# Kernel optimization log

Measured on AMD Instinct MI355X. Metric: run time of the kernel, lower is better.

## Reference

```python
import jax, jax.numpy as jnp
import numpy as np

NUM_USER = 30000
NUM_ITEM = 30000
N = NUM_USER + NUM_ITEM
DIM = 64          # dim_latent
HID = 4 * DIM     # MLP hidden = 4*dim_latent
E_PAIRS = 500000  # user-item interactions; symmetrized -> 2*E_PAIRS edges
K = 10            # sampling (user-graph neighbors)
B = 2048          # batch_size
DV, DA, DT = 1024, 128, 100


def setup_inputs() -> dict:
    key = jax.random.key(0)
    ks = jax.random.split(key, 24)
    src = jax.random.randint(ks[0], (E_PAIRS,), 0, NUM_USER)
    dst = jax.random.randint(ks[1], (E_PAIRS,), NUM_USER, N)
    # symmetrize like torch.cat((edge, edge[[1,0]]), dim=1)
    edge_index = jnp.stack([jnp.concatenate([src, dst]),
                            jnp.concatenate([dst, src])])  # [2, 2*E_PAIRS]

    def lin_w(k, o, i):
        s = 1.0 / np.sqrt(i)
        return jax.random.uniform(k, (o, i), minval=-s, maxval=s, dtype=jnp.float32)

    return {
        "user_nodes": jax.random.randint(ks[2], (B,), 0, NUM_USER),
        "pos_item_nodes": jax.random.randint(ks[3], (B,), NUM_USER, N),
        "neg_item_nodes": jax.random.randint(ks[4], (B,), NUM_USER, N),
        "user_graph": jax.random.randint(ks[5], (NUM_USER, K), 0, NUM_USER),
        "edge_index": edge_index,
        "user_weight_matrix": jax.nn.softmax(jax.random.normal(ks[6], (NUM_USER, K), dtype=jnp.float32), axis=-1),
        "v_feat": jax.random.normal(ks[7], (NUM_ITEM, DV), dtype=jnp.float32),
        "a_feat": jax.random.normal(ks[8], (NUM_ITEM, DA), dtype=jnp.float32),
        "t_feat": jax.random.normal(ks[9], (NUM_ITEM, DT), dtype=jnp.float32),
        "v_pref": 0.1 * jax.random.normal(ks[10], (NUM_USER, DIM), dtype=jnp.float32),
        "a_pref": 0.1 * jax.random.normal(ks[11], (NUM_USER, DIM), dtype=jnp.float32),
        "t_pref": 0.1 * jax.random.normal(ks[12], (NUM_USER, DIM), dtype=jnp.float32),
        "v_W1": lin_w(ks[13], HID, DV), "v_b1": jnp.zeros((HID,), jnp.float32),
        "v_W2": lin_w(ks[14], DIM, HID), "v_b2": jnp.zeros((DIM,), jnp.float32),
        "a_W1": lin_w(ks[15], HID, DA), "a_b1": jnp.zeros((HID,), jnp.float32),
        "a_W2": lin_w(ks[16], DIM, HID), "a_b2": jnp.zeros((DIM,), jnp.float32),
        "t_W1": lin_w(ks[17], HID, DT), "t_b1": jnp.zeros((HID,), jnp.float32),
        "t_W2": lin_w(ks[18], DIM, HID), "t_b2": jnp.zeros((DIM,), jnp.float32),
        "weight_u": jax.nn.softmax(jax.random.normal(ks[19], (NUM_USER, 3, 1), dtype=jnp.float32), axis=1),
    }


def _l2norm(x):
    # F.normalize(x): rowwise L2 with eps=1e-12
    return x / jnp.maximum(jnp.linalg.norm(x, axis=-1, keepdims=True), 1e-12)


def _gcn_conv(x, src, dst, dinv):
    # Base_gcn(aggr='add'): out[i] = sum_{e: dst_e=i} dinv[src_e]*dinv[dst_e]*x[src_e]
    norm = dinv[src] * dinv[dst]
    return jax.ops.segment_sum(norm[:, None] * x[src], dst, num_segments=N)


def _modality(feat, pref, W1, b1, W2, b2, src, dst, dinv):
    # GCN.forward (Movielens branch, dim_latent=64)
    temp = jax.nn.leaky_relu(feat @ W1.T + b1) @ W2.T + b2  # MLP_1(leaky_relu(MLP(f)))
    x = _l2norm(jnp.concatenate([pref, temp], axis=0))       # [N, DIM]
    h = _gcn_conv(x, src, dst, dinv)
    h1 = _gcn_conv(h, src, dst, dinv)
    return h + x + h1


def reference(user_nodes, pos_item_nodes, neg_item_nodes, user_graph, edge_index,
              user_weight_matrix, v_feat, a_feat, t_feat,
              v_pref, a_pref, t_pref,
              v_W1, v_b1, v_W2, v_b2,
              a_W1, a_b1, a_W2, a_b2,
              t_W1, t_b1, t_W2, t_b2, weight_u):
    src, dst = edge_index[0], edge_index[1]
    deg = jax.ops.segment_sum(jnp.ones_like(src, dtype=jnp.float32), src, num_segments=N)
    dinv = jnp.where(deg > 0, deg ** -0.5, 0.0)

    v_rep = _modality(v_feat, v_pref, v_W1, v_b1, v_W2, v_b2, src, dst, dinv)
    a_rep = _modality(a_feat, a_pref, a_W1, a_b1, a_W2, a_b2, src, dst, dinv)
    t_rep = _modality(t_feat, t_pref, t_W1, t_b1, t_W2, t_b2, src, dst, dinv)

    representation = (v_rep + a_rep + t_rep) / 3.0
    # weighted_sum construction: per-user learned modality weights [U,3,1]
    user_stack = jnp.stack([v_rep[:NUM_USER], a_rep[:NUM_USER], t_rep[:NUM_USER]], axis=2)  # [U, D, 3]
    user_rep = jnp.einsum('udm,umo->ud', user_stack, weight_u)
    item_rep = representation[NUM_USER:]

    # User_Graph_sample: weighted sum over k sampled user neighbors
    h_u1 = jnp.einsum('uk,ukd->ud', user_weight_matrix, user_rep[user_graph])
    user_rep = user_rep + h_u1

    result = jnp.concatenate([user_rep, item_rep], axis=0)  # [N, DIM]
    u = result[user_nodes]
    pos_scores = jnp.sum(u * result[pos_item_nodes], axis=1)
    neg_scores = jnp.sum(u * result[neg_item_nodes], axis=1)
    return pos_scores, neg_scores
```

## Files before the change

### kernel.cpp

```cpp
#include <hip/hip_runtime.h>
#include <hip/hip_bf16.h>
#include <math.h>

#define NUSER 30000
#define NITEM 30000
#define NN    60000
#define NE    1000000
#define DIMV  64
#define XW    192
#define HIDW  256
#define NB    2048
#define KNB   10
#define MPAD  30080
#define NCH   235

typedef __attribute__((ext_vector_type(8))) short bf16x8;
typedef __attribute__((ext_vector_type(4))) float f32x4;

__device__ __forceinline__ short f2bf(float f) {
    union { float f; unsigned u; } v; v.f = f;
    unsigned r = v.u + 0x7fff + ((v.u >> 16) & 1);
    return (short)(r >> 16);
}
__device__ __forceinline__ float bflo(unsigned v) { return __int_as_float(v << 16); }
__device__ __forceinline__ float bfhi(unsigned v) { return __int_as_float(v & 0xffff0000u); }
__device__ __forceinline__ unsigned pack2(float a, float b) {
    return (unsigned)(unsigned short)f2bf(a) | ((unsigned)(unsigned short)f2bf(b) << 16);
}
__device__ __forceinline__ void async16(void* lds, const void* g) {
    __builtin_amdgcn_global_load_lds(
        (const __attribute__((address_space(1))) unsigned*)g,
        (__attribute__((address_space(3))) unsigned*)lds, 16, 0, 0);
}

__global__ void k_deg(const int* __restrict__ src, unsigned* __restrict__ deg) {
    int e = blockIdx.x * blockDim.x + threadIdx.x;
    if (e < NE) atomicAdd(&deg[src[e]], 1u);
}
__global__ void k_dinv(const unsigned* __restrict__ deg, float* __restrict__ dinv) {
    int i = blockIdx.x * blockDim.x + threadIdx.x;
    if (i < NN) { unsigned d = deg[i]; dinv[i] = d ? rsqrtf((float)d) : 0.f; }
}
__global__ __launch_bounds__(256)
void k_bsum(const unsigned* __restrict__ deg, int* __restrict__ bsum) {
    __shared__ int red[4];
    int g = blockIdx.x * 256 + threadIdx.x;
    int v = (g < NN) ? (int)deg[g] : 0;
    for (int o = 32; o > 0; o >>= 1) v += __shfl_down(v, o);
    int lane = threadIdx.x & 63, wave = threadIdx.x >> 6;
    if (lane == 0) red[wave] = v;
    __syncthreads();
    if (threadIdx.x == 0) bsum[blockIdx.x] = red[0] + red[1] + red[2] + red[3];
}
__global__ __launch_bounds__(256)
void k_bscan(const int* __restrict__ bsum, int* __restrict__ bscan) {
    __shared__ int s[256];
    int t = threadIdx.x;
    int v = (t < NCH) ? bsum[t] : 0;
    s[t] = v;
    __syncthreads();
    for (int o = 1; o < 256; o <<= 1) {
        int u = (t >= o) ? s[t - o] : 0;
        __syncthreads();
        s[t] += u;
        __syncthreads();
    }
    if (t < NCH) bscan[t] = s[t] - v;
}
__global__ __launch_bounds__(256)
void k_rowptr(const unsigned* __restrict__ deg, const int* __restrict__ bscan,
              int* __restrict__ rowptr) {
    __shared__ int s[256];
    int g = blockIdx.x * 256 + threadIdx.x, t = threadIdx.x;
    int v = (g < NN) ? (int)deg[g] : 0;
    s[t] = v;
    __syncthreads();
    for (int o = 1; o < 256; o <<= 1) {
        int u = (t >= o) ? s[t - o] : 0;
        __syncthreads();
        s[t] += u;
        __syncthreads();
    }
    int base = bscan[blockIdx.x];
    if (g < NN) rowptr[g] = base + s[t] - v;
    if (g == NN - 1) rowptr[NN] = base + s[t];
}
__global__ void k_fill(const int* __restrict__ src, const int* __restrict__ dst,
                       const float* __restrict__ dinv, const int* __restrict__ rowptr,
                       unsigned* __restrict__ cursor, int2* __restrict__ csr) {
    int e = blockIdx.x * blockDim.x + threadIdx.x;
    if (e >= NE) return;
    int s = src[e], d = dst[e];
    int pos = (int)atomicAdd(&cursor[d], 1u);
    int2 ew;
    ew.x = s;
    ew.y = __float_as_int(dinv[s] * dinv[d]);
    csr[rowptr[d] + pos] = ew;
}

struct CvtArgs { const float* src[6]; short* dst[6]; };
__constant__ __device__ const int C8PRE[7]  = {0,32768,36864,40960,43008,45056,47104};
__constant__ __device__ const int C8SH[6]   = {7,4,4,5,5,5};
__constant__ __device__ const int C8COLS[6] = {1024,128,100,256,256,256};
__constant__ __device__ const int C8ROWS[6] = {256,256,256,64,64,64};
#define CVT8_TOTAL 47104

__global__ __launch_bounds__(256)
void k_convert(CvtArgs a) {
    int cid = blockIdx.x * 256 + threadIdx.x;
    if (cid >= CVT8_TOTAL) return;
    int j = 0;
    while (cid >= C8PRE[j + 1]) ++j;
    int local = cid - C8PRE[j];
    int sh = C8SH[j];
    int r = local >> sh;
    int col = (local & ((1 << sh) - 1)) * 8;
    int cols = C8COLS[j];
    bf16x8 o = (bf16x8)0;
    if (r < C8ROWS[j]) {
        const float* s = a.src[j] + (size_t)r * cols + col;
        if (col + 8 <= cols) {
            float4 f0 = *(const float4*)s;
            float4 f1 = *(const float4*)(s + 4);
            o[0] = f2bf(f0.x); o[1] = f2bf(f0.y); o[2] = f2bf(f0.z); o[3] = f2bf(f0.w);
            o[4] = f2bf(f1.x); o[5] = f2bf(f1.y); o[6] = f2bf(f1.z); o[7] = f2bf(f1.w);
        } else {
            #pragma unroll
            for (int q = 0; q < 8; ++q)
                if (col + q < cols) o[q] = f2bf(s[q]);
        }
    }
    *(bf16x8*)(a.dst[j] + ((size_t)r << (sh + 3)) + col) = o;
}

__device__ __forceinline__ bf16x8 ldfrag(const short* lds, int row, int kbyte) {
    int off = (row * 128 + kbyte) ^ ((row & 7) << 4);
    return *(const bf16x8*)((const char*)lds + off);
}
__device__ __forceinline__ bf16x8 ldfrag512(const short* lds, int row, int kbyte) {
    int off = (row * 512 + kbyte) ^ ((row & 7) << 4);
    return *(const bf16x8*)((const char*)lds + off);
}
#define STAGE_TILE512(SMEM, BASEPTR, LDK, ROWOFF, K0, NITERS)                       \
    _Pragma("unroll")                                                                \
    for (int i_ = 0; i_ < (NITERS); ++i_) {                                          \
        int c_ = i_ * 512 + tid;                                                     \
        int r_ = c_ >> 3, slot_ = c_ & 7;                                            \
        int ss_ = slot_ ^ (r_ & 7);                                                  \
        const char* gp_ = (const char*)((BASEPTR) + (size_t)((ROWOFF) + r_) * (LDK)  \
                                        + (K0)) + ss_ * 16;                          \
        async16(&(SMEM)[c_ * 8], gp_);                                               \
    }

struct G12Args { const float* A[3]; const short* W1[3]; const float* b1[3];
                 const short* W2[3]; const float* b2[3]; int K[3]; int Ksrc[3]; };
__global__ __launch_bounds__(512)
void gemm12_mfma(G12Args g, float* __restrict__ X, short* __restrict__ Xb) {
    __shared__ __align__(16) float sAf[64 * 64];
    __shared__ __align__(16) short sB[256 * 64];
    short* sHid = sB;
    int m = blockIdx.z;
    int K  = g.K[m];
    int Ks = g.Ksrc[m];
    const float* A  = g.A[m];
    const short* W1 = g.W1[m];
    int tid = threadIdx.x;
    int lane = tid & 63, wave = tid >> 6;
    int wr2 = wave & 1, wc2 = wave >> 1;
    int lane15 = lane & 15, lhi = lane >> 4;
    int row0 = blockIdx.x * 64;
    int nt = K >> 6;
    f32x4 acc[2][4] = {};
    for (int t = 0; t < nt; ++t) {
        int k0 = t * 64;
        #pragma unroll
        for (int i_ = 0; i_ < 2; ++i_) {
            int c_ = i_ * 512 + tid;
            int r_ = c_ >> 4, slot = c_ & 15;
            int ss = slot ^ (r_ & 7);
            int grow = row0 + r_;
            if (grow >= NITEM) grow = NITEM - 1;
            int col = k0 + ss * 4;
            if (col + 4 > Ks) col = 0;
            async16(&sAf[c_ * 4], A + (size_t)grow * Ks + col);
        }
        STAGE_TILE512(sB, W1, K, 0, k0, 4)
        __syncthreads();
        #pragma unroll
        for (int ks = 0; ks < 2; ++ks) {
            bf16x8 a[2], b[4];
            #pragma unroll
            for (int mi = 0; mi < 2; ++mi) {
                int row = wr2 * 32 + mi * 16 + lane15;
                int cb = (ks * 32 + lhi * 8) * 4;
                int base = row * 256;
                int sw = (row & 7) << 4;
                f32x4 lo = *(const f32x4*)((const char*)sAf + ((base + cb) ^ sw));
                f32x4 hi = *(const f32x4*)((const char*)sAf + ((base + cb + 16) ^ sw));
                unsigned p0, p1, p2, p3;
                asm("v_cvt_pk_bf16_f32 %0, %1, %2" : "=v"(p0) : "v"(lo.x), "v"(lo.y));
                asm("v_cvt_pk_bf16_f32 %0, %1, %2" : "=v"(p1) : "v"(lo.z), "v"(lo.w));
                asm("v_cvt_pk_bf16_f32 %0, %1, %2" : "=v"(p2) : "v"(hi.x), "v"(hi.y));
                asm("v_cvt_pk_bf16_f32 %0, %1, %2" : "=v"(p3) : "v"(hi.z), "v"(hi.w));
                union { unsigned u[4]; bf16x8 v; } cvt;
                cvt.u[0] = p0; cvt.u[1] = p1; cvt.u[2] = p2; cvt.u[3] = p3;
                a[mi] = cvt.v;
            }
            int kb = ks * 64 + lhi * 16;
            #pragma unroll
            for (int ni = 0; ni < 4; ++ni) b[ni] = ldfrag(sB, wc2 * 64 + ni * 16 + lane15, kb);
            #pragma unroll
            for (int mi = 0; mi < 2; ++mi)
                #pragma unroll
                for (int ni = 0; ni < 4; ++ni)
                    acc[mi][ni] = __builtin_amdgcn_mfma_f32_16x16x32_bf16(a[mi], b[ni], acc[mi][ni], 0, 0, 0);
        }
        __syncthreads();
    }
    const float* b1 = g.b1[m];
    #pragma unroll
    for (int mi = 0; mi < 2; ++mi) {
        int rh0 = wr2 * 32 + mi * 16 + lhi * 4;
        #pragma unroll
        for (int ni = 0; ni < 4; ++ni) {
            int ch = wc2 * 64 + ni * 16 + lane15;
            float bv = b1[ch];
            #pragma unroll
            for (int r = 0; r < 4; ++r) {
                float v = acc[mi][ni][r] + bv;
                v = v > 0.f ? v : 0.01f * v;
                int rh = rh0 + r;
                int off = (rh * 512 + ch * 2) ^ ((rh & 7) << 4);
                *(short*)((char*)sHid + off) = f2bf(v);
            }
        }
    }
    __syncthreads();
    if (wave < 4) {
        const short* W2 = g.W2[m];
        const short* bp2 = W2 + (size_t)lane15 * HIDW + lhi * 8;
        f32x4 acc2[4] = {};
        #pragma unroll
        for (int k0 = 0; k0 < HIDW; k0 += 32) {
            bf16x8 a2 = ldfrag512(sHid, wave * 16 + lane15, k0 * 2 + lhi * 16);
            #pragma unroll
            for (int ni = 0; ni < 4; ++ni) {
                bf16x8 b2 = *(const bf16x8*)(bp2 + (size_t)ni * 16 * HIDW + k0);
                acc2[ni] = __builtin_amdgcn_mfma_f32_16x16x32_bf16(a2, b2, acc2[ni], 0, 0, 0);
            }
        }
        const float* b2 = g.b2[m];
        float v2[4][4];
        float sumsq[4] = {};
        #pragma unroll
        for (int ni = 0; ni < 4; ++ni) {
            float bv = b2[ni * 16 + lane15];
            #pragma unroll
            for (int r = 0; r < 4; ++r) {
                float x = acc2[ni][r] + bv;
                v2[ni][r] = x;
                sumsq[r] += x * x;
            }
        }
        #pragma unroll
        for (int r = 0; r < 4; ++r) {
            float s = sumsq[r];
            s += __shfl_xor(s, 1); s += __shfl_xor(s, 2);
            s += __shfl_xor(s, 4); s += __shfl_xor(s, 8);
            sumsq[r] = 1.f / fmaxf(sqrtf(s), 1e-12f);
        }
        int grow0 = row0 + wave * 16 + lhi * 4;
        #pragma unroll
        for (int r = 0; r < 4; ++r) {
            int grow = grow0 + r;
            if (grow < NITEM) {
                float sc = sumsq[r];
                size_t o = (size_t)(NUSER + grow) * XW + m * DIMV;
                #pragma unroll
                for (int ni = 0; ni < 4; ++ni) {
                    float val = v2[ni][r] * sc;
                    X[o + ni * 16 + lane15] = val;
                    Xb[o + ni * 16 + lane15] = f2bf(val);
                }
            }
        }
    }
}

__global__ void k_users_norm(const float* __restrict__ vp, const float* __restrict__ ap,
                             const float* __restrict__ tp, float* __restrict__ X,
                             short* __restrict__ Xb) {
    int gw = (blockIdx.x * blockDim.x + threadIdx.x) >> 6;
    int lane = threadIdx.x & 63;
    if (gw >= NUSER * 3) return;
    int u = gw / 3, m = gw % 3;
    const float* p = (m == 0) ? vp : (m == 1) ? ap : tp;
    float v = p[(size_t)u * DIMV + lane];
    float s = v * v;
    for (int o = 32; o > 0; o >>= 1) s += __shfl_xor(s, o);
    float sc = 1.f / fmaxf(sqrtf(s), 1e-12f);
    size_t o = (size_t)u * XW + m * DIMV + lane;
    float val = v * sc;
    X[o] = val;
    Xb[o] = f2bf(val);
}

template<int MODE>
__global__ __launch_bounds__(256)
void k_spmm(const int* __restrict__ rowptr, const int2* __restrict__ csr,
            const short* __restrict__ INB, const float* __restrict__ Xf,
            float* __restrict__ OUTf, short* __restrict__ OUTB) {
    int n = blockIdx.x * 4 + (threadIdx.x >> 6);
    int l = threadIdx.x & 63;
    if (n >= NN) return;
    int lo = rowptr[n], hi = rowptr[n + 1];
    int lc = l < 48 ? l : 47;
    float f0 = 0.f, f1 = 0.f, f2 = 0.f, f3 = 0.f;
    for (int base = lo; base < hi; base += 64) {
        int idx = base + l;
        int2 e = (idx < hi) ? csr[idx] : make_int2(0, 0);
        int m = hi - base; if (m > 64) m = 64;
        int j = 0;
        for (; j + 4 <= m; j += 4) {
            int s0 = __builtin_amdgcn_readlane(e.x, j + 0);
            int s1 = __builtin_amdgcn_readlane(e.x, j + 1);
            int s2 = __builtin_amdgcn_readlane(e.x, j + 2);
            int s3 = __builtin_amdgcn_readlane(e.x, j + 3);
            float w0 = __int_as_float(__builtin_amdgcn_readlane(e.y, j + 0));
            float w1 = __int_as_float(__builtin_amdgcn_readlane(e.y, j + 1));
            float w2 = __int_as_float(__builtin_amdgcn_readlane(e.y, j + 2));
            float w3 = __int_as_float(__builtin_amdgcn_readlane(e.y, j + 3));
            uint2 v0 = ((const uint2*)(INB + (size_t)s0 * XW))[lc];
            uint2 v1 = ((const uint2*)(INB + (size_t)s1 * XW))[lc];
            uint2 v2 = ((const uint2*)(INB + (size_t)s2 * XW))[lc];
            uint2 v3 = ((const uint2*)(INB + (size_t)s3 * XW))[lc];
            f0 += w0 * bflo(v0.x); f1 += w0 * bfhi(v0.x);
            f2 += w0 * bflo(v0.y); f3 += w0 * bfhi(v0.y);
            f0 += w1 * bflo(v1.x); f1 += w1 * bfhi(v1.x);
            f2 += w1 * bflo(v1.y); f3 += w1 * bfhi(v1.y);
            f0 += w2 * bflo(v2.x); f1 += w2 * bfhi(v2.x);
            f2 += w2 * bflo(v2.y); f3 += w2 * bfhi(v2.y);
            f0 += w3 * bflo(v3.x); f1 += w3 * bfhi(v3.x);
            f2 += w3 * bflo(v3.y); f3 += w3 * bfhi(v3.y);
        }
        for (; j < m; ++j) {
            int s0 = __builtin_amdgcn_readlane(e.x, j);
            float w0 = __int_as_float(__builtin_amdgcn_readlane(e.y, j));
            uint2 v0 = ((const uint2*)(INB + (size_t)s0 * XW))[lc];
            f0 += w0 * bflo(v0.x); f1 += w0 * bfhi(v0.x);
            f2 += w0 * bflo(v0.y); f3 += w0 * bfhi(v0.y);
        }
    }
    if (MODE == 1) {
        float4 xv = ((const float4*)(Xf + (size_t)n * XW))[lc];
        uint2 hb = ((const uint2*)(INB + (size_t)n * XW))[lc];
        f0 += xv.x + bflo(hb.x); f1 += xv.y + bfhi(hb.x);
        f2 += xv.z + bflo(hb.y); f3 += xv.w + bfhi(hb.y);
    }
    if (l < 48) {
        if (MODE == 0) {
            uint2 ob;
            ob.x = pack2(f0, f1);
            ob.y = pack2(f2, f3);
            ((uint2*)(OUTB + (size_t)n * XW))[l] = ob;
        } else {
            ((float4*)(OUTf + (size_t)n * XW))[l] = make_float4(f0, f1, f2, f3);
        }
    }
}

__global__ void k_combine(const float* __restrict__ REP, const float* __restrict__ wu,
                          float* __restrict__ UR, float* __restrict__ RES) {
    int t = blockIdx.x * blockDim.x + threadIdx.x;
    if (t >= NN * DIMV) return;
    int n = t >> 6, d = t & 63;
    const float* r = REP + (size_t)n * XW;
    float r0 = r[d], r1 = r[DIMV + d], r2 = r[2 * DIMV + d];
    if (n < NUSER) {
        float w0 = wu[n * 3 + 0], w1 = wu[n * 3 + 1], w2 = wu[n * 3 + 2];
        UR[(size_t)n * DIMV + d] = r0 * w0 + r1 * w1 + r2 * w2;
    } else {
        RES[(size_t)n * DIMV + d] = (r0 + r1 + r2) * (1.f / 3.f);
    }
}
__global__ void k_usergraph(const float* __restrict__ UR, const int* __restrict__ g,
                            const float* __restrict__ w, float* __restrict__ RES) {
    int t = blockIdx.x * blockDim.x + threadIdx.x;
    if (t >= NUSER * DIMV) return;
    int n = t >> 6, d = t & 63;
    float acc = UR[(size_t)n * DIMV + d];
    for (int k = 0; k < KNB; ++k) {
        int nb = g[n * KNB + k];
        acc += w[n * KNB + k] * UR[(size_t)nb * DIMV + d];
    }
    RES[(size_t)n * DIMV + d] = acc;
}
__global__ void k_scores(const float* __restrict__ RES, const int* __restrict__ un,
                         const int* __restrict__ pn, const int* __restrict__ nn,
                         float* __restrict__ out) {
    int gw = (blockIdx.x * blockDim.x + threadIdx.x) >> 6;
    int lane = threadIdx.x & 63;
    if (gw >= NB) return;
    int u = un[gw], p = pn[gw], ng = nn[gw];
    float uv = RES[(size_t)u * DIMV + lane];
    float ps = uv * RES[(size_t)p * DIMV + lane];
    float ns = uv * RES[(size_t)ng * DIMV + lane];
    for (int o = 32; o > 0; o >>= 1) {
        ps += __shfl_xor(ps, o);
        ns += __shfl_xor(ns, o);
    }
    if (lane == 0) { out[gw] = ps; out[NB + gw] = ns; }
}

extern "C" void kernel_launch(void* const* d_in, const int* in_sizes, int n_in,
                              void* d_out, int out_size, void* d_ws, size_t ws_size,
                              hipStream_t stream) {
    const int*   un    = (const int*)d_in[0];
    const int*   pn    = (const int*)d_in[1];
    const int*   ngn   = (const int*)d_in[2];
    const int*   ug    = (const int*)d_in[3];
    const int*   eidx  = (const int*)d_in[4];
    const float* uwm   = (const float*)d_in[5];
    const float* feats[3] = { (const float*)d_in[6], (const float*)d_in[7], (const float*)d_in[8] };
    const float* prefs[3] = { (const float*)d_in[9], (const float*)d_in[10], (const float*)d_in[11] };
    const float* W1[3] = { (const float*)d_in[12], (const float*)d_in[16], (const float*)d_in[20] };
    const float* b1[3] = { (const float*)d_in[13], (const float*)d_in[17], (const float*)d_in[21] };
    const float* W2[3] = { (const float*)d_in[14], (const float*)d_in[18], (const float*)d_in[22] };
    const float* b2[3] = { (const float*)d_in[15], (const float*)d_in[19], (const float*)d_in[23] };
    const float* wu    = (const float*)d_in[24];
    float* out = (float*)d_out;

    const int* esrc = eidx;
    const int* edst = eidx + NE;

    char* ws = (char*)d_ws;
    size_t off = 0;
    auto alloc = [&](size_t bytes) { void* p = ws + off; off = (off + bytes + 255) & ~(size_t)255; return p; };
    unsigned* deg    = (unsigned*)alloc(NN * 4);
    float*    dinv   = (float*)alloc(NN * 4);
    int*      rowptr = (int*)alloc((NN + 1) * 4);
    int*      bsum   = (int*)alloc(NCH * 4);
    int*      bscan  = (int*)alloc(NCH * 4);
    int2*     csr    = (int2*)alloc((size_t)NE * 8);
    float*    X      = (float*)alloc((size_t)NN * XW * 4);
    short*    Xb     = (short*)alloc((size_t)NN * XW * 2);
    char* region2 = (char*)alloc((size_t)3 * MPAD * HIDW * 2);
    float* RES = (float*)region2;
    float* UR  = (float*)(region2 + (size_t)NN * DIMV * 4 + 40960);
    short* Hb  = (short*)(region2 + (size_t)NN * DIMV * 4 + 40960 + (size_t)NUSER * DIMV * 4);
    short* w1b = (short*)alloc((size_t)256 * 1280 * 2);
    short* w1s[3] = { w1b, w1b + 256 * 1024, w1b + 256 * (1024 + 128) };
    short* w2b = (short*)alloc((size_t)3 * 64 * HIDW * 2);
    short* w2s[3] = { w2b, w2b + 64 * HIDW, w2b + 2 * 64 * HIDW };

    CvtArgs ca;
    ca.src[0] = W1[0]; ca.src[1] = W1[1]; ca.src[2] = W1[2];
    ca.src[3] = W2[0]; ca.src[4] = W2[1]; ca.src[5] = W2[2];
    ca.dst[0] = w1s[0]; ca.dst[1] = w1s[1]; ca.dst[2] = w1s[2];
    ca.dst[3] = w2s[0]; ca.dst[4] = w2s[1]; ca.dst[5] = w2s[2];
    k_convert<<<(CVT8_TOTAL + 255) / 256, 256, 0, stream>>>(ca);

    hipMemsetAsync(deg, 0, NN * 4, stream);
    k_deg<<<(NE + 255) / 256, 256, 0, stream>>>(esrc, deg);
    k_dinv<<<(NN + 255) / 256, 256, 0, stream>>>(deg, dinv);
    k_bsum<<<NCH, 256, 0, stream>>>(deg, bsum);
    k_bscan<<<1, 256, 0, stream>>>(bsum, bscan);
    k_rowptr<<<NCH, 256, 0, stream>>>(deg, bscan, rowptr);
    hipMemsetAsync(deg, 0, NN * 4, stream);
    k_fill<<<(NE + 255) / 256, 256, 0, stream>>>(esrc, edst, dinv, rowptr, deg, csr);

    G12Args g12;
    for (int m = 0; m < 3; ++m) {
        g12.A[m] = feats[m]; g12.W1[m] = w1s[m]; g12.b1[m] = b1[m];
        g12.W2[m] = w2s[m];  g12.b2[m] = b2[m];
    }
    g12.K[0] = 1024; g12.K[1] = 128; g12.K[2] = 128;
    g12.Ksrc[0] = 1024; g12.Ksrc[1] = 128; g12.Ksrc[2] = 100;
    gemm12_mfma<<<dim3(MPAD / 64, 1, 3), 512, 0, stream>>>(g12, X, Xb);
    k_users_norm<<<(NUSER * 3 * 64 + 255) / 256, 256, 0, stream>>>(prefs[0], prefs[1], prefs[2], X, Xb);

    k_spmm<0><<<(NN + 3) / 4, 256, 0, stream>>>(rowptr, csr, Xb, nullptr, nullptr, Hb);

    k_spmm<1><<<(NN + 3) / 4, 256, 0, stream>>>(rowptr, csr, Hb, X, X, nullptr);

    k_combine<<<(NN * DIMV + 255) / 256, 256, 0, stream>>>(X, wu, UR, RES);
    k_usergraph<<<(NUSER * DIMV + 255) / 256, 256, 0, stream>>>(UR, ug, uwm, RES);
    k_scores<<<(NB * 64 + 255) / 256, 256, 0, stream>>>(RES, un, pn, ngn, out);
}
```

Baseline: 328.3 us.

## Double-buffer A and W1 tiles in first GEMM loop with async prefetch

The first-layer MLP GEMM kernel now keeps two LDS buffers for the A (fp32 features) and W1 tiles and issues the async loads for tile t+1 before computing tile t. Partial vmcnt waits replace full barriers so global loads can overlap MFMA work. The cost is doubled LDS use (96KB per block), which may lower occupancy, plus hand-managed waitcnt counts that must match the number of outstanding async copies.

```diff
diff --git a/kernel.cpp b/kernel.cpp
--- a/kernel.cpp
+++ b/kernel.cpp
@@ -141,24 +141,17 @@
     int off = (row * 512 + kbyte) ^ ((row & 7) << 4);
     return *(const bf16x8*)((const char*)lds + off);
 }
-#define STAGE_TILE512(SMEM, BASEPTR, LDK, ROWOFF, K0, NITERS)                       \
-    _Pragma("unroll")                                                                \
-    for (int i_ = 0; i_ < (NITERS); ++i_) {                                          \
-        int c_ = i_ * 512 + tid;                                                     \
-        int r_ = c_ >> 3, slot_ = c_ & 7;                                            \
-        int ss_ = slot_ ^ (r_ & 7);                                                  \
-        const char* gp_ = (const char*)((BASEPTR) + (size_t)((ROWOFF) + r_) * (LDK)  \
-                                        + (K0)) + ss_ * 16;                          \
-        async16(&(SMEM)[c_ * 8], gp_);                                               \
-    }
 
 struct G12Args { const float* A[3]; const short* W1[3]; const float* b1[3];
                  const short* W2[3]; const float* b2[3]; int K[3]; int Ksrc[3]; };
 __global__ __launch_bounds__(512)
 void gemm12_mfma(G12Args g, float* __restrict__ X, short* __restrict__ Xb) {
-    __shared__ __align__(16) float sAf[64 * 64];
-    __shared__ __align__(16) short sB[256 * 64];
-    short* sHid = sB;
+    __shared__ __align__(16) char smem[98304];
+    float* sAf0 = (float*)smem;
+    float* sAf1 = (float*)(smem + 16384);
+    short* sBb0 = (short*)(smem + 32768);
+    short* sBb1 = (short*)(smem + 65536);
+    short* sHid = sBb0;
     int m = blockIdx.z;
     int K  = g.K[m];
     int Ks = g.Ksrc[m];
@@ -170,8 +163,8 @@
     int lane15 = lane & 15, lhi = lane >> 4;
     int row0 = blockIdx.x * 64;
     int nt = K >> 6;
-    f32x4 acc[2][4] = {};
-    for (int t = 0; t < nt; ++t) {
+
+    auto stageA = [&](float* dst, int t) {
         int k0 = t * 64;
         #pragma unroll
         for (int i_ = 0; i_ < 2; ++i_) {
@@ -182,10 +175,22 @@
             if (grow >= NITEM) grow = NITEM - 1;
             int col = k0 + ss * 4;
             if (col + 4 > Ks) col = 0;
-            async16(&sAf[c_ * 4], A + (size_t)grow * Ks + col);
-        }
-        STAGE_TILE512(sB, W1, K, 0, k0, 4)
-        __syncthreads();
+            async16(&dst[c_ * 4], A + (size_t)grow * Ks + col);
+        }
+    };
+    auto stageB = [&](short* dst, int t) {
+        int k0 = t * 64;
+        #pragma unroll
+        for (int i_ = 0; i_ < 4; ++i_) {
+            int c_ = i_ * 512 + tid;
+            int r_ = c_ >> 3, slot_ = c_ & 7;
+            int ss_ = slot_ ^ (r_ & 7);
+            const char* gp_ = (const char*)(W1 + (size_t)r_ * K + k0) + ss_ * 16;
+            async16(&dst[c_ * 8], gp_);
+        }
+    };
+    f32x4 acc[2][4] = {};
+    auto compute = [&](const float* sAf, const short* sBb) {
         #pragma unroll
         for (int ks = 0; ks < 2; ++ks) {
             bf16x8 a[2], b[4];
@@ -208,14 +213,32 @@
             }
             int kb = ks * 64 + lhi * 16;
             #pragma unroll
-            for (int ni = 0; ni < 4; ++ni) b[ni] = ldfrag(sB, wc2 * 64 + ni * 16 + lane15, kb);
+            for (int ni = 0; ni < 4; ++ni) b[ni] = ldfrag(sBb, wc2 * 64 + ni * 16 + lane15, kb);
             #pragma unroll
             for (int mi = 0; mi < 2; ++mi)
                 #pragma unroll
                 for (int ni = 0; ni < 4; ++ni)
                     acc[mi][ni] = __builtin_amdgcn_mfma_f32_16x16x32_bf16(a[mi], b[ni], acc[mi][ni], 0, 0, 0);
         }
-        __syncthreads();
+    };
+
+    stageA(sAf0, 0);
+    stageB(sBb0, 0);
+    for (int t = 0; t < nt; ++t) {
+        int cur = t & 1;
+        bool more = (t + 1 < nt);
+        if (more) {
+            if (cur == 0) { stageA(sAf1, t + 1); stageB(sBb1, t + 1); }
+            else          { stageA(sAf0, t + 1); stageB(sBb0, t + 1); }
+            asm volatile("s_waitcnt vmcnt(6)" ::: "memory");
+        } else {
+            asm volatile("s_waitcnt vmcnt(0)" ::: "memory");
+        }
+        __builtin_amdgcn_s_barrier();
+        __builtin_amdgcn_sched_barrier(0);
+        compute(cur == 0 ? sAf0 : sAf1, cur == 0 ? sBb0 : sBb1);
+        asm volatile("s_waitcnt lgkmcnt(0)" ::: "memory");
+        __builtin_amdgcn_s_barrier();
     }
     const float* b1 = g.b1[m];
     #pragma unroll
```

After: 342.9 us. +4.5%, slower.
